# Kernel optimization log

Hardware: AMD Instinct MI355X
Metric: run time of the kernel (lower is better)

Reference implementation:

```python
import jax, jax.numpy as jnp
import numpy as np

DIM = 1024
HEADS = 16
HEAD_DIM = DIM // HEADS
SCALE = HEAD_DIM ** -0.5


def setup_inputs() -> dict:
    key = jax.random.key(0)
    ks = jax.random.split(key, 9)
    B, S, D = 2, 2048, DIM
    std = 1.0 / np.sqrt(D)
    Z = jax.random.normal(ks[0], (B, S, D), dtype=jnp.float32)
    Wq = jax.random.uniform(ks[1], (D, D), jnp.float32, -std, std)
    bq = jax.random.uniform(ks[2], (D,), jnp.float32, -std, std)
    Wk = jax.random.uniform(ks[3], (D, D), jnp.float32, -std, std)
    bk = jax.random.uniform(ks[4], (D,), jnp.float32, -std, std)
    Wv = jax.random.uniform(ks[5], (D, D), jnp.float32, -std, std)
    bv = jax.random.uniform(ks[6], (D,), jnp.float32, -std, std)
    Wo = jax.random.uniform(ks[7], (D, D), jnp.float32, -std, std)
    bo = jax.random.uniform(ks[8], (D,), jnp.float32, -std, std)
    return {"Z": Z, "Wq": Wq, "bq": bq, "Wk": Wk, "bk": bk,
            "Wv": Wv, "bv": bv, "Wo": Wo, "bo": bo}


def reference(Z, Wq, bq, Wk, bk, Wv, bv, Wo, bo):
    B, S, D = Z.shape
    H, Hd = HEADS, HEAD_DIM
    # torch Linear: y = x @ W.T + b
    Q = (Z @ Wq.T + bq).reshape(B, S, H, Hd).transpose(0, 2, 1, 3)  # [B,H,S,Hd]
    K = (Z @ Wk.T + bk).reshape(B, S, H, Hd).transpose(0, 2, 1, 3)
    V = (Z @ Wv.T + bv).reshape(B, S, H, Hd).transpose(0, 2, 1, 3)
    scores = jnp.einsum('bhqd,bhkd->bhqk', Q, K) * SCALE  # [B,H,S,S]
    weights = jax.nn.softmax(scores, axis=-1)
    weights = jnp.nan_to_num(weights, nan=0.0)
    # dropout=0.0 -> identity (eval mode)
    out = jnp.einsum('bhqk,bhkd->bhqd', weights, V)  # [B,H,S,Hd]
    out = out.transpose(0, 2, 1, 3).reshape(B, S, D)
    return out @ Wo.T + bo
```

## Files before the change

### kernel.cpp

```cpp
#include <hip/hip_runtime.h>
#include <hip/hip_bf16.h>
#include <stdint.h>

typedef unsigned short u16;
typedef __bf16 bf16x8 __attribute__((ext_vector_type(8)));
typedef float f32x4 __attribute__((ext_vector_type(4)));
typedef float f32x16 __attribute__((ext_vector_type(16)));

#define D_MODEL 1024
#define SEQ     2048
#define NB      2
#define NH      16
#define HD      64
#define M_TOT   (NB*SEQ)
#define QSCALE  (0.125f * 1.44269504088896f)
#define DEFER_THR 8.0f

__device__ __forceinline__ u16 f2bf(float f) {
  union { __bf16 b; u16 u; } cv; cv.b = (__bf16)f; return cv.u;
}
__device__ __forceinline__ float exp2_fast(float x) {
  return __builtin_amdgcn_exp2f(x);
}

__device__ __forceinline__ void async_copy16(void* lds_dst, const void* gsrc) {
  __builtin_amdgcn_global_load_lds(
      (const __attribute__((address_space(1))) unsigned int*)gsrc,
      (__attribute__((address_space(3))) unsigned int*)lds_dst, 16, 0, 0);
}

__global__ void cvt_all(const float* __restrict__ Z,  const float* __restrict__ Wq,
                        const float* __restrict__ Wk, const float* __restrict__ Wv,
                        const float* __restrict__ Wo,
                        u16* __restrict__ Zb,  u16* __restrict__ Wqb,
                        u16* __restrict__ Wkb, u16* __restrict__ Wvb,
                        u16* __restrict__ Wob)
{
  int i = blockIdx.x * 256 + threadIdx.x;
  const float* src; u16* dst; int off;
  if (i < (1 << 20)) { src = Z; dst = Zb; off = i; }
  else {
    int j = i - (1 << 20);
    int seg = j >> 18; off = j & ((1 << 18) - 1);
    src = (seg == 0) ? Wq : (seg == 1) ? Wk : (seg == 2) ? Wv : Wo;
    dst = (seg == 0) ? Wqb : (seg == 1) ? Wkb : (seg == 2) ? Wvb : Wob;
  }
  float4 v = reinterpret_cast<const float4*>(src)[off];
  ushort4 o;
  o.x = f2bf(v.x); o.y = f2bf(v.y); o.z = f2bf(v.z); o.w = f2bf(v.w);
  reinterpret_cast<ushort4*>(dst)[off] = o;
}

template<int F32OUT, int TRANSV>
__global__ __launch_bounds__(512, 2)
void gemm256(const u16* __restrict__ A,
             const u16* __restrict__ B0, const u16* __restrict__ B1, const u16* __restrict__ B2,
             const float* __restrict__ bias0, const float* __restrict__ bias1, const float* __restrict__ bias2,
             void* __restrict__ C0, void* __restrict__ C1, void* __restrict__ C2,
             float s0f, float s1f, float s2f,
             int M, int N, int K)
{
  (void)M;
  const int z = blockIdx.z;
  const u16* Bt = (z == 0) ? B0 : ((z == 1) ? B1 : B2);
  const float* bias = (z == 0) ? bias0 : ((z == 1) ? bias1 : bias2);
  void* Cout = (z == 0) ? C0 : ((z == 1) ? C1 : C2);
  const float oscl = (z == 0) ? s0f : ((z == 1) ? s1f : s2f);
  const bool vswap = TRANSV && (z == 2);

  extern __shared__ u16 smem[];
  char* La = (char*)smem;
  char* Lb = (char*)smem + 65536;

  const int tid = threadIdx.x;
  const int w = tid >> 6, lane = tid & 63;
  const int l15 = lane & 15, lhi = lane >> 4;
  const int m0 = blockIdx.y * 256, n0 = blockIdx.x * 256;
  const int wm = w >> 2, wn = w & 3;

  f32x4 acc[8][4] = {};

  int aoff[4], boff[4];
  #pragma unroll
  for (int i = 0; i < 4; ++i) {
    const int c = i*512 + tid;
    const int row = c >> 3;
    const int sl  = c & 7;
    const int sg  = sl ^ (row & 7);
    aoff[i] = (m0 + row) * K + sg*8;
    boff[i] = (n0 + row) * K + sg*8;
  }
  const int ldsoff0 = (0*512 + w*64)*16, ldsoff1 = (1*512 + w*64)*16,
            ldsoff2 = (2*512 + w*64)*16, ldsoff3 = (3*512 + w*64)*16;

  auto stage = [&](int buf, int kt) {
    const int ko = kt << 6;
    const int bb = buf * 32768;
    async_copy16(La + bb + ldsoff0, A  + (size_t)(aoff[0] + ko));
    async_copy16(Lb + bb + ldsoff0, Bt + (size_t)(boff[0] + ko));
    async_copy16(La + bb + ldsoff1, A  + (size_t)(aoff[1] + ko));
    async_copy16(Lb + bb + ldsoff1, Bt + (size_t)(boff[1] + ko));
    async_copy16(La + bb + ldsoff2, A  + (size_t)(aoff[2] + ko));
    async_copy16(Lb + bb + ldsoff2, Bt + (size_t)(boff[2] + ko));
    async_copy16(La + bb + ldsoff3, A  + (size_t)(aoff[3] + ko));
    async_copy16(Lb + bb + ldsoff3, Bt + (size_t)(boff[3] + ko));
  };

  const int s0 = lhi ^ (l15 & 7);
  const int abase = (wm*128 + l15)*128 + s0*16;
  const int bbase = (wn*64  + l15)*128 + s0*16;

  auto compute = [&](int buf) {
    const int bb = buf * 32768;
    #pragma unroll
    for (int ks = 0; ks < 2; ++ks) {
      const int pa = bb + (abase ^ (ks << 6));
      const int pb = bb + (bbase ^ (ks << 6));
      bf16x8 bf[4];
      #pragma unroll
      for (int ni = 0; ni < 4; ++ni)
        bf[ni] = *reinterpret_cast<const bf16x8*>(Lb + pb + ni*2048);
      #pragma unroll
      for (int mi = 0; mi < 8; ++mi) {
        bf16x8 af = *reinterpret_cast<const bf16x8*>(La + pa + mi*2048);
        if (vswap) {
          #pragma unroll
          for (int ni = 0; ni < 4; ++ni)
            acc[mi][ni] = __builtin_amdgcn_mfma_f32_16x16x32_bf16(bf[ni], af, acc[mi][ni], 0, 0, 0);
        } else {
          #pragma unroll
          for (int ni = 0; ni < 4; ++ni)
            acc[mi][ni] = __builtin_amdgcn_mfma_f32_16x16x32_bf16(af, bf[ni], acc[mi][ni], 0, 0, 0);
        }
      }
    }
  };

  const int nt = K >> 6;
  stage(0, 0);
  stage(1, 1);
  for (int t = 0; t < nt; ++t) {
    const int cb = t & 1;
    if (t + 1 < nt) { asm volatile("s_waitcnt vmcnt(8)" ::: "memory"); }
    else            { asm volatile("s_waitcnt vmcnt(0)" ::: "memory"); }
    __builtin_amdgcn_sched_barrier(0);
    __builtin_amdgcn_s_barrier();
    __builtin_amdgcn_sched_barrier(0);
    compute(cb);
    __builtin_amdgcn_sched_barrier(0);
    __builtin_amdgcn_s_barrier();
    if (t + 2 < nt) stage(cb, t + 2);
  }

  if (vswap) {
    #pragma unroll
    for (int mi = 0; mi < 8; ++mi) {
      const int sglob = m0 + wm*128 + mi*16 + l15;
      const int b2 = sglob >> 11, s = sglob & (SEQ - 1);
      #pragma unroll
      for (int ni = 0; ni < 4; ++ni) {
        #pragma unroll
        for (int r = 0; r < 4; ++r) {
          const int dglob = n0 + wn*64 + ni*16 + (lhi << 2) + r;
          const int hh = dglob >> 6, dd = dglob & 63;
          const float v = acc[mi][ni][r] + bias[dglob];
          reinterpret_cast<u16*>(Cout)[((size_t)(b2*NH + hh)*HD + dd)*SEQ + s] = f2bf(v);
        }
      }
    }
  } else {
    #pragma unroll
    for (int mi = 0; mi < 8; ++mi) {
      const int rowb = m0 + wm*128 + mi*16 + (lhi << 2);
      #pragma unroll
      for (int ni = 0; ni < 4; ++ni) {
        const int col = n0 + wn*64 + ni*16 + l15;
        const float bb = bias[col];
        #pragma unroll
        for (int r = 0; r < 4; ++r) {
          const float v = (acc[mi][ni][r] + bb) * oscl;
          if (F32OUT)
            reinterpret_cast<float*>(Cout)[(size_t)(rowb + r) * N + col] = v;
          else
            reinterpret_cast<u16*>(Cout)[(size_t)(rowb + r) * N + col] = f2bf(v);
        }
      }
    }
  }
}

__global__ __launch_bounds__(256, 2)
void attn32(const u16* __restrict__ Qb, const u16* __restrict__ Kb,
            const u16* __restrict__ Vt, u16* __restrict__ Ob)
{
  __shared__ u16 vt[3][64*64];
  __shared__ u16 kt[3][64*64];

  const int tid = threadIdx.x;
  const int w = tid >> 6, lane = tid & 63;
  const int l31 = lane & 31, hi = lane >> 5;
  const int bh = blockIdx.y, b = bh >> 4, h = bh & 15;
  const int qrow = blockIdx.x * 128 + w * 32 + l31;

  bf16x8 qf[4];
  {
    const u16* qp = Qb + (size_t)(b*SEQ + qrow) * D_MODEL + h*HD + hi*8;
    #pragma unroll
    for (int kc = 0; kc < 4; ++kc)
      qf[kc] = *reinterpret_cast<const bf16x8*>(qp + kc*16);
  }

  const u16* Vtg = Vt + (size_t)bh * HD * SEQ;
  const u16* Kg  = Kb + (size_t)(b*SEQ) * D_MODEL + h*HD;

  float mrun = -1e30f, lrun = 0.f;
  f32x16 o0 = {}, o1 = {};

  auto stageKV = [&](int buf, int kv0) {
    #pragma unroll
    for (int i = 0; i < 2; ++i) {
      const int c = i*256 + tid;
      const int d = c >> 3;
      const int sl = c & 7;
      const int sg = sl ^ (d & 7);
      async_copy16((char*)vt[buf] + (size_t)(i*256 + w*64)*16,
                   (const char*)(Vtg + (size_t)d*SEQ + kv0 + sg*8));
    }
    #pragma unroll
    for (int i = 0; i < 2; ++i) {
      const int c = i*256 + tid;
      const int key = c >> 3;
      const int sl = c & 7;
      const int sg = sl ^ (key & 7);
      async_copy16((char*)kt[buf] + (size_t)(i*256 + w*64)*16,
                   (const char*)(Kg + (size_t)(kv0 + key)*D_MODEL + sg*8));
    }
  };

  const int nt = SEQ / 64;
  stageKV(0, 0);
  stageKV(1, 64);

  for (int t = 0; t < nt; ++t) {
    const int cb = t % 3;
    if (t + 2 < nt) stageKV((t + 2) % 3, (t + 2) * 64);
    if (t + 2 < nt)      { asm volatile("s_waitcnt vmcnt(8)" ::: "memory"); }
    else if (t + 1 < nt) { asm volatile("s_waitcnt vmcnt(4)" ::: "memory"); }
    else                 { asm volatile("s_waitcnt vmcnt(0)" ::: "memory"); }
    __builtin_amdgcn_sched_barrier(0);
    __builtin_amdgcn_s_barrier();
    __builtin_amdgcn_sched_barrier(0);

    f32x16 s0 = {}, s1 = {};
    {
      const char* kbp = (const char*)kt[cb];
      #pragma unroll
      for (int kc = 0; kc < 4; ++kc) {
        const int sw = (kc*2 + hi) ^ (l31 & 7);
        bf16x8 ka0 = *reinterpret_cast<const bf16x8*>(kbp + (size_t)(l31*8 + sw)*16);
        s0 = __builtin_amdgcn_mfma_f32_32x32x16_bf16(ka0, qf[kc], s0, 0, 0, 0);
        bf16x8 ka1 = *reinterpret_cast<const bf16x8*>(kbp + (size_t)((l31+32)*8 + sw)*16);
        s1 = __builtin_amdgcn_mfma_f32_32x32x16_bf16(ka1, qf[kc], s1, 0, 0, 0);
      }
    }

    float tmax = s0[0];
    #pragma unroll
    for (int r = 1; r < 16; ++r) tmax = fmaxf(tmax, s0[r]);
    #pragma unroll
    for (int r = 0; r < 16; ++r) tmax = fmaxf(tmax, s1[r]);
    tmax = fmaxf(tmax, __shfl_xor(tmax, 32));
    if (!__all(tmax - mrun <= DEFER_THR)) {
      const float mnew = fmaxf(mrun, tmax);
      const float a = exp2_fast(mrun - mnew);
      lrun *= a;
      #pragma unroll
      for (int r = 0; r < 16; ++r) { o0[r] *= a; o1[r] *= a; }
      mrun = mnew;
    }
    float rs = 0.f;
    #pragma unroll
    for (int r = 0; r < 16; ++r) { s0[r] = exp2_fast(s0[r] - mrun); rs += s0[r]; }
    #pragma unroll
    for (int r = 0; r < 16; ++r) { s1[r] = exp2_fast(s1[r] - mrun); rs += s1[r]; }
    rs += __shfl_xor(rs, 32);
    lrun += rs;

    unsigned pwA[2][8];
    #pragma unroll
    for (int a4 = 0; a4 < 4; ++a4)
      #pragma unroll
      for (int zz = 0; zz < 2; ++zz) {
        pwA[0][a4*2+zz] = (unsigned)f2bf(s0[4*a4+2*zz]) | ((unsigned)f2bf(s0[4*a4+2*zz+1]) << 16);
        pwA[1][a4*2+zz] = (unsigned)f2bf(s1[4*a4+2*zz]) | ((unsigned)f2bf(s1[4*a4+2*zz+1]) << 16);
      }

    const char* vb = (const char*)vt[cb];
    #pragma unroll
    for (int ks = 0; ks < 4; ++ks) {
      const int kb = ks >> 1, sm = ks & 1;
      unsigned keep0 = hi ? pwA[kb][(2*sm+1)*2+0] : pwA[kb][(2*sm)*2+0];
      unsigned keep1 = hi ? pwA[kb][(2*sm+1)*2+1] : pwA[kb][(2*sm)*2+1];
      unsigned send0 = hi ? pwA[kb][(2*sm)*2+0]   : pwA[kb][(2*sm+1)*2+0];
      unsigned send1 = hi ? pwA[kb][(2*sm)*2+1]   : pwA[kb][(2*sm+1)*2+1];
      unsigned recv0 = (unsigned)__shfl_xor((int)send0, 32);
      unsigned recv1 = (unsigned)__shfl_xor((int)send1, 32);
      union { bf16x8 f; unsigned u[4]; } pf;
      pf.u[0] = hi ? recv0 : keep0;
      pf.u[1] = hi ? recv1 : keep1;
      pf.u[2] = hi ? keep0 : recv0;
      pf.u[3] = hi ? keep1 : recv1;

      const int slg = ks*2 + hi;
      const int sw  = slg ^ (l31 & 7);
      bf16x8 va0 = *reinterpret_cast<const bf16x8*>(vb + (size_t)(l31*8 + sw)*16);
      bf16x8 va1 = *reinterpret_cast<const bf16x8*>(vb + (size_t)((l31+32)*8 + sw)*16);

      o0 = __builtin_amdgcn_mfma_f32_32x32x16_bf16(va0, pf.f, o0, 0, 0, 0);
      o1 = __builtin_amdgcn_mfma_f32_32x32x16_bf16(va1, pf.f, o1, 0, 0, 0);
    }

    __builtin_amdgcn_sched_barrier(0);
    __builtin_amdgcn_s_barrier();
  }

  const float inv = 1.0f / lrun;
  u16* op = Ob + (size_t)(b*SEQ + qrow) * D_MODEL + h*HD;
  #pragma unroll
  for (int a4 = 0; a4 < 4; ++a4) {
    ushort4 v0, v1;
    v0.x = f2bf(o0[4*a4+0]*inv); v0.y = f2bf(o0[4*a4+1]*inv);
    v0.z = f2bf(o0[4*a4+2]*inv); v0.w = f2bf(o0[4*a4+3]*inv);
    v1.x = f2bf(o1[4*a4+0]*inv); v1.y = f2bf(o1[4*a4+1]*inv);
    v1.z = f2bf(o1[4*a4+2]*inv); v1.w = f2bf(o1[4*a4+3]*inv);
    *reinterpret_cast<ushort4*>(op + 8*a4 + 4*hi)      = v0;
    *reinterpret_cast<ushort4*>(op + 32 + 8*a4 + 4*hi) = v1;
  }
}

extern "C" void kernel_launch(void* const* d_in, const int* in_sizes, int n_in,
                              void* d_out, int out_size, void* d_ws, size_t ws_size,
                              hipStream_t stream)
{
  (void)in_sizes; (void)n_in; (void)out_size;
  const float* Z  = (const float*)d_in[0];
  const float* Wq = (const float*)d_in[1];
  const float* bq = (const float*)d_in[2];
  const float* Wk = (const float*)d_in[3];
  const float* bk = (const float*)d_in[4];
  const float* Wv = (const float*)d_in[5];
  const float* bv = (const float*)d_in[6];
  const float* Wo = (const float*)d_in[7];
  const float* bo = (const float*)d_in[8];
  float* out = (float*)d_out;

  const size_t needed = (size_t)(M_TOT*D_MODEL)*2*5 + (size_t)(D_MODEL*D_MODEL)*2*4;
  if (ws_size < needed) return;

  u16* Zb  = (u16*)d_ws;
  u16* Wqb = Zb  + (size_t)M_TOT*D_MODEL;
  u16* Wkb = Wqb + (size_t)D_MODEL*D_MODEL;
  u16* Wvb = Wkb + (size_t)D_MODEL*D_MODEL;
  u16* Wob = Wvb + (size_t)D_MODEL*D_MODEL;
  u16* Qb  = Wob + (size_t)D_MODEL*D_MODEL;
  u16* Kb  = Qb  + (size_t)M_TOT*D_MODEL;
  u16* Vt  = Kb  + (size_t)M_TOT*D_MODEL;
  u16* Ab  = Vt  + (size_t)M_TOT*D_MODEL;

  cvt_all<<<dim3(8192), 256, 0, stream>>>(Z, Wq, Wk, Wv, Wo, Zb, Wqb, Wkb, Wvb, Wob);

  const size_t lds_bytes = 131072;

  dim3 gproj(D_MODEL/256, M_TOT/256, 3);
  gemm256<0,1><<<gproj, 512, lds_bytes, stream>>>(Zb, Wqb, Wkb, Wvb, bq, bk, bv,
                                                  (void*)Qb, (void*)Kb, (void*)Vt,
                                                  QSCALE, 1.0f, 1.0f,
                                                  M_TOT, D_MODEL, D_MODEL);

  dim3 gattn(SEQ/128, NB*NH);
  attn32<<<gattn, 256, 0, stream>>>(Qb, Kb, Vt, Ab);

  dim3 gout(D_MODEL/256, M_TOT/256, 1);
  gemm256<1,0><<<gout, 512, lds_bytes, stream>>>(Ab, Wob, Wob, Wob, bo, bo, bo,
                                                 (void*)out, (void*)out, (void*)out,
                                                 1.0f, 1.0f, 1.0f,
                                                 M_TOT, D_MODEL, D_MODEL);
}
```

Baseline: 247.3 us.

## Interleave GEMM prefetch with MFMA quarters and swizzle block order

Restructures the projection GEMM main loop. It now issues the next k-tile's global-to-LDS copies in four slices, one per quarter of the MFMA work, and waits with vmcnt(0) at the top of each iteration, replacing the old two-ahead prefetch with coarse waits. It raises wave priority around MFMA bursts and remaps block IDs into eight interleaved groups to change L2 reuse. The cost is more barriers per k-tile (four instead of two) and a prefetch depth of only one tile, which may expose memory latency.

```diff
diff --git a/kernel.cpp b/kernel.cpp
--- a/kernel.cpp
+++ b/kernel.cpp
@@ -75,7 +75,12 @@
   const int tid = threadIdx.x;
   const int w = tid >> 6, lane = tid & 63;
   const int l15 = lane & 15, lhi = lane >> 4;
-  const int m0 = blockIdx.y * 256, n0 = blockIdx.x * 256;
+
+  int id = blockIdx.x + gridDim.x * blockIdx.y;
+  const int n2 = gridDim.x * gridDim.y;
+  id = (id & 7) * (n2 >> 3) + (id >> 3);
+  const int bx = id % gridDim.x, by = id / gridDim.x;
+  const int m0 = by * 256, n0 = bx * 256;
   const int wm = w >> 2, wn = w & 3;
 
   f32x4 acc[8][4] = {};
@@ -90,66 +95,92 @@
     aoff[i] = (m0 + row) * K + sg*8;
     boff[i] = (n0 + row) * K + sg*8;
   }
-  const int ldsoff0 = (0*512 + w*64)*16, ldsoff1 = (1*512 + w*64)*16,
-            ldsoff2 = (2*512 + w*64)*16, ldsoff3 = (3*512 + w*64)*16;
-
-  auto stage = [&](int buf, int kt) {
+  int ldsoff[4];
+  #pragma unroll
+  for (int i = 0; i < 4; ++i) ldsoff[i] = (i*512 + w*64)*16;
+
+  auto stage_pair = [&](int j, int buf, int kt) {
     const int ko = kt << 6;
     const int bb = buf * 32768;
-    async_copy16(La + bb + ldsoff0, A  + (size_t)(aoff[0] + ko));
-    async_copy16(Lb + bb + ldsoff0, Bt + (size_t)(boff[0] + ko));
-    async_copy16(La + bb + ldsoff1, A  + (size_t)(aoff[1] + ko));
-    async_copy16(Lb + bb + ldsoff1, Bt + (size_t)(boff[1] + ko));
-    async_copy16(La + bb + ldsoff2, A  + (size_t)(aoff[2] + ko));
-    async_copy16(Lb + bb + ldsoff2, Bt + (size_t)(boff[2] + ko));
-    async_copy16(La + bb + ldsoff3, A  + (size_t)(aoff[3] + ko));
-    async_copy16(Lb + bb + ldsoff3, Bt + (size_t)(boff[3] + ko));
+    if (j == 0) {
+      async_copy16(Lb + bb + ldsoff[0], Bt + (size_t)(boff[0] + ko));
+      async_copy16(Lb + bb + ldsoff[1], Bt + (size_t)(boff[1] + ko));
+    } else if (j == 1) {
+      async_copy16(Lb + bb + ldsoff[2], Bt + (size_t)(boff[2] + ko));
+      async_copy16(Lb + bb + ldsoff[3], Bt + (size_t)(boff[3] + ko));
+    } else if (j == 2) {
+      async_copy16(La + bb + ldsoff[0], A + (size_t)(aoff[0] + ko));
+      async_copy16(La + bb + ldsoff[1], A + (size_t)(aoff[1] + ko));
+    } else {
+      async_copy16(La + bb + ldsoff[2], A + (size_t)(aoff[2] + ko));
+      async_copy16(La + bb + ldsoff[3], A + (size_t)(aoff[3] + ko));
+    }
   };
 
-  const int s0 = lhi ^ (l15 & 7);
-  const int abase = (wm*128 + l15)*128 + s0*16;
-  const int bbase = (wn*64  + l15)*128 + s0*16;
-
-  auto compute = [&](int buf) {
-    const int bb = buf * 32768;
-    #pragma unroll
-    for (int ks = 0; ks < 2; ++ks) {
-      const int pa = bb + (abase ^ (ks << 6));
-      const int pb = bb + (bbase ^ (ks << 6));
-      bf16x8 bf[4];
-      #pragma unroll
-      for (int ni = 0; ni < 4; ++ni)
-        bf[ni] = *reinterpret_cast<const bf16x8*>(Lb + pb + ni*2048);
-      #pragma unroll
-      for (int mi = 0; mi < 8; ++mi) {
-        bf16x8 af = *reinterpret_cast<const bf16x8*>(La + pa + mi*2048);
-        if (vswap) {
+  const int sl0 = lhi ^ (l15 & 7);
+  const int abase = (wm*128 + l15)*128 + sl0*16;
+  const int bbase = (wn*64  + l15)*128 + sl0*16;
+
+  const int nt = K >> 6;
+
+  #pragma unroll
+  for (int j = 0; j < 4; ++j) stage_pair(j, 0, 0);
+
+  int cur = 0;
+  for (int t = 0; t < nt; ++t) {
+    const int bb = cur * 32768;
+    const bool pf = (t + 1 < nt);
+    bf16x8 Bf[4][2];
+
+    #pragma unroll
+    for (int q = 0; q < 4; ++q) {
+      if (q == 0) {
+        asm volatile("s_waitcnt vmcnt(0)" ::: "memory");
+        __builtin_amdgcn_sched_barrier(0);
+        __builtin_amdgcn_s_barrier();
+        __builtin_amdgcn_sched_barrier(0);
+      } else {
+        __builtin_amdgcn_s_barrier();
+        __builtin_amdgcn_sched_barrier(0);
+      }
+      if (pf) stage_pair(q, cur ^ 1, t + 1);
+
+      if (q == 0) {
+        #pragma unroll
+        for (int ni = 0; ni < 4; ++ni)
           #pragma unroll
-          for (int ni = 0; ni < 4; ++ni)
-            acc[mi][ni] = __builtin_amdgcn_mfma_f32_16x16x32_bf16(bf[ni], af, acc[mi][ni], 0, 0, 0);
-        } else {
-          #pragma unroll
-          for (int ni = 0; ni < 4; ++ni)
-            acc[mi][ni] = __builtin_amdgcn_mfma_f32_16x16x32_bf16(af, bf[ni], acc[mi][ni], 0, 0, 0);
+          for (int ks = 0; ks < 2; ++ks)
+            Bf[ni][ks] = *reinterpret_cast<const bf16x8*>(Lb + bb + ((bbase + ni*2048) ^ (ks << 6)));
+      }
+      bf16x8 Af[2][2];
+      #pragma unroll
+      for (int mm = 0; mm < 2; ++mm)
+        #pragma unroll
+        for (int ks = 0; ks < 2; ++ks)
+          Af[mm][ks] = *reinterpret_cast<const bf16x8*>(La + bb + ((abase + (q*2+mm)*2048) ^ (ks << 6)));
+
+      asm volatile("s_waitcnt lgkmcnt(0)" ::: "memory");
+      __builtin_amdgcn_sched_barrier(0);
+      __builtin_amdgcn_s_setprio(1);
+      #pragma unroll
+      for (int ks = 0; ks < 2; ++ks)
+        #pragma unroll
+        for (int mm = 0; mm < 2; ++mm) {
+          const int mi = q*2 + mm;
+          if (vswap) {
+            #pragma unroll
+            for (int ni = 0; ni < 4; ++ni)
+              acc[mi][ni] = __builtin_amdgcn_mfma_f32_16x16x32_bf16(Bf[ni][ks], Af[mm][ks], acc[mi][ni], 0, 0, 0);
+          } else {
+            #pragma unroll
+            for (int ni = 0; ni < 4; ++ni)
+              acc[mi][ni] = __builtin_amdgcn_mfma_f32_16x16x32_bf16(Af[mm][ks], Bf[ni][ks], acc[mi][ni], 0, 0, 0);
+          }
         }
-      }
-    }
-  };
-
-  const int nt = K >> 6;
-  stage(0, 0);
-  stage(1, 1);
-  for (int t = 0; t < nt; ++t) {
-    const int cb = t & 1;
-    if (t + 1 < nt) { asm volatile("s_waitcnt vmcnt(8)" ::: "memory"); }
-    else            { asm volatile("s_waitcnt vmcnt(0)" ::: "memory"); }
-    __builtin_amdgcn_sched_barrier(0);
-    __builtin_amdgcn_s_barrier();
-    __builtin_amdgcn_sched_barrier(0);
-    compute(cb);
-    __builtin_amdgcn_sched_barrier(0);
-    __builtin_amdgcn_s_barrier();
-    if (t + 2 < nt) stage(cb, t + 2);
+      __builtin_amdgcn_s_setprio(0);
+      __builtin_amdgcn_sched_barrier(0);
+    }
+    cur ^= 1;
   }
 
   if (vswap) {
@@ -175,10 +206,10 @@
       #pragma unroll
       for (int ni = 0; ni < 4; ++ni) {
         const int col = n0 + wn*64 + ni*16 + l15;
-        const float bb = bias[col];
+        const float bb2 = bias[col];
         #pragma unroll
         for (int r = 0; r < 4; ++r) {
-          const float v = (acc[mi][ni][r] + bb) * oscl;
+          const float v = (acc[mi][ni][r] + bb2) * oscl;
           if (F32OUT)
             reinterpret_cast<float*>(Cout)[(size_t)(rowb + r) * N + col] = v;
           else
```

Measured after the change: 218.4 us. -11.7%, faster.
